# Performance work log

Measured on AMD Instinct MI355X. Metric: run time of the kernel, lower is better.

## Reference

```python
import jax, jax.numpy as jnp
import numpy as np

B = 4096   # per-view batch size
D = 256    # projection dim
TEMPERATURE = 0.1
EPS = 1e-12  # F.normalize eps


def setup_inputs() -> dict:
    key = jax.random.key(0)
    kq, kk = jax.random.split(key)
    features_q = jax.random.normal(kq, (B, D), dtype=jnp.float32)
    features_k = jax.random.normal(kk, (B, D), dtype=jnp.float32)
    return {"features_q": features_q, "features_k": features_k}


def _neg_index_matrix(n):
    # Static (numpy) construction of the per-row negative column indices:
    # row i keeps all columns except i (diagonal) and its positive partner.
    rows = np.arange(n)
    partner = (rows + n // 2) % n
    cols = np.broadcast_to(np.arange(n), (n, n))
    keep = (cols != rows[:, None]) & (cols != partner[:, None])
    return cols[keep].reshape(n, n - 2), partner


def reference(features_q, features_k):
    f = jnp.concatenate([features_q, features_k], axis=0)      # [2B, D]
    norm = jnp.maximum(jnp.linalg.norm(f, axis=1, keepdims=True), EPS)
    f = f / norm
    sim = f @ f.T                                              # [2B, 2B]

    n = 2 * B
    neg_idx_np, partner_np = _neg_index_matrix(n)
    rows = jnp.arange(n)
    partner = jnp.asarray(partner_np)
    pos = sim[rows, partner]                                   # [2B]
    neg = jnp.take_along_axis(sim, jnp.asarray(neg_idx_np), axis=1)  # [2B, 2B-2]

    logits = jnp.concatenate([pos[:, None], neg], axis=1) / TEMPERATURE
    # CrossEntropyLoss with label 0 for every row, mean reduction:
    loss = jnp.mean(jax.nn.logsumexp(logits, axis=1) - logits[:, 0])
    return loss
```

## Files before the change

### kernel.cpp

```cpp
#include <hip/hip_runtime.h>
#include <hip/hip_bf16.h>
#include <math.h>

#define N_TOTAL 8192
#define D_DIM   256
#define INV_T   10.0f
#define BM 128
#define BN 128
#define BK 32
#define K_ITERS (D_DIM / BK)
#define NT 64
#define N_TILES (NT * (NT + 1) / 2)

typedef __bf16 bf16_8 __attribute__((ext_vector_type(8)));
typedef float  f32x4  __attribute__((ext_vector_type(4)));

typedef const __attribute__((address_space(1))) unsigned int* gptr_t;
typedef __attribute__((address_space(3))) unsigned int*       lptr_t;

__device__ __forceinline__ void gload16(const void* g, void* l) {
    __builtin_amdgcn_global_load_lds((gptr_t)g, (lptr_t)l, 16, 0, 0);
}

__device__ __forceinline__ unsigned short f2bf(float f) {
    unsigned int u = __float_as_uint(f);
    return (unsigned short)((u + 0x7FFFu + ((u >> 16) & 1u)) >> 16);
}

__global__ __launch_bounds__(256) void normalize_kernel(
    const float* __restrict__ q, const float* __restrict__ k,
    unsigned short* __restrict__ F, float* __restrict__ out)
{
    if (blockIdx.x == 0 && threadIdx.x == 0) out[0] = 0.f;
    int row  = blockIdx.x * 4 + (threadIdx.x >> 6);
    int lane = threadIdx.x & 63;
    const float* src = (row < 4096) ? (q + (size_t)row * D_DIM)
                                    : (k + (size_t)(row - 4096) * D_DIM);
    float4 v = ((const float4*)src)[lane];
    float ss = v.x*v.x + v.y*v.y + v.z*v.z + v.w*v.w;
    #pragma unroll
    for (int off = 32; off > 0; off >>= 1) ss += __shfl_xor(ss, off, 64);
    float inv = 1.0f / fmaxf(sqrtf(ss), 1e-12f);
    ushort4 o;
    o.x = f2bf(v.x * inv); o.y = f2bf(v.y * inv);
    o.z = f2bf(v.z * inv); o.w = f2bf(v.w * inv);
    ((ushort4*)(F + (size_t)row * D_DIM))[lane] = o;
}

__device__ __forceinline__ int tri_off(int x) { return x * NT - (x * (x - 1)) / 2; }

__global__ __launch_bounds__(256) void simloss_gemm(
    const __hip_bfloat16* __restrict__ F,
    float* __restrict__ partial, float* __restrict__ pos)
{
    __shared__ __hip_bfloat16 As[2][BM * BK];
    __shared__ __hip_bfloat16 Bs[2][BN * BK];
    __shared__ float s_row[BM];
    __shared__ float s_col[BN];

    int b  = blockIdx.x;
    int bx = (int)(64.5f - sqrtf(64.5f * 64.5f - 2.0f * (float)b));
    if (bx < 0) bx = 0; if (bx > NT - 1) bx = NT - 1;
    while (bx > 0 && tri_off(bx) > b) --bx;
    while (bx < NT - 1 && tri_off(bx + 1) <= b) ++bx;
    const int by = bx + (b - tri_off(bx));
    const bool is_diag = (bx == by);

    const int i0 = bx * BM;
    const int j0 = by * BN;
    const int tid  = threadIdx.x;
    const int wave = tid >> 6;
    const int lane = tid & 63;
    const int wm = (wave & 1) * 64;
    const int wn = (wave >> 1) * 64;
    const int g  = lane >> 4;
    const int cj = lane & 15;
    const int srow  = lane >> 2;
    const int squar = (lane & 3) * 8;

    if (tid < BM) { s_row[tid] = 0.f; s_col[tid] = 0.f; }

    f32x4 acc[4][4];
    #pragma unroll
    for (int a = 0; a < 4; ++a)
        #pragma unroll
        for (int c = 0; c < 4; ++c)
            acc[a][c] = (f32x4){0.f, 0.f, 0.f, 0.f};

    #define STAGE(buf, kk)                                                            \
        _Pragma("unroll")                                                             \
        for (int p = 0; p < 2; ++p) {                                                 \
            gload16(F + (size_t)(i0 + wave * 32 + p * 16 + srow) * D_DIM + (kk) + squar, \
                    &As[buf][(wave * 32 + p * 16) * BK]);                             \
            gload16(F + (size_t)(j0 + wave * 32 + p * 16 + srow) * D_DIM + (kk) + squar, \
                    &Bs[buf][(wave * 32 + p * 16) * BK]);                             \
        }

    STAGE(0, 0);
    int cur = 0;
    for (int kk = 0; kk < K_ITERS; ++kk) {
        __builtin_amdgcn_s_barrier();
        if (kk + 1 < K_ITERS) {
            STAGE(cur ^ 1, (kk + 1) * BK);
            asm volatile("s_waitcnt vmcnt(4)" ::: "memory");
        } else {
            asm volatile("s_waitcnt vmcnt(0)" ::: "memory");
        }

        bf16_8 a[4], bfr[4];
        #pragma unroll
        for (int t = 0; t < 4; ++t) {
            a[t]   = *(const bf16_8*)(&As[cur][(wm + t * 16 + cj) * BK + g * 8]);
            bfr[t] = *(const bf16_8*)(&Bs[cur][(wn + t * 16 + cj) * BK + g * 8]);
        }
        #pragma unroll
        for (int ti = 0; ti < 4; ++ti)
            #pragma unroll
            for (int tj = 0; tj < 4; ++tj)
                acc[ti][tj] = __builtin_amdgcn_mfma_f32_16x16x32_bf16(
                    a[ti], bfr[tj], acc[ti][tj], 0, 0, 0);

        cur ^= 1;
    }
    #undef STAGE

    float colsum[4] = {0.f, 0.f, 0.f, 0.f};
    #pragma unroll
    for (int ti = 0; ti < 4; ++ti) {
        #pragma unroll
        for (int r = 0; r < 4; ++r) {
            const int i = i0 + wm + ti * 16 + g * 4 + r;
            const int partner = (i + 4096) & (N_TOTAL - 1);
            float esum = 0.f;
            #pragma unroll
            for (int tj = 0; tj < 4; ++tj) {
                const int j = j0 + wn + tj * 16 + cj;
                const float v = acc[ti][tj][r];
                float e = __expf(v * INV_T);
                if (is_diag && j == i) e = 0.f;
                if (!is_diag && j == partner) {
                    pos[i] = v; pos[j] = v;
                }
                esum += e;
                colsum[tj] += e;
            }
            #pragma unroll
            for (int off = 1; off < 16; off <<= 1)
                esum += __shfl_xor(esum, off, 64);
            if (cj == 0) atomicAdd(&s_row[wm + ti * 16 + g * 4 + r], esum);
        }
    }
    if (!is_diag) {
        #pragma unroll
        for (int tj = 0; tj < 4; ++tj) {
            float cs = colsum[tj];
            cs += __shfl_xor(cs, 16, 64);
            cs += __shfl_xor(cs, 32, 64);
            if (g == 0) atomicAdd(&s_col[wn + tj * 16 + cj], cs);
        }
    }
    __syncthreads();

    if (tid < BM) {
        partial[(size_t)by * N_TOTAL + i0 + tid] = s_row[tid];
    } else if (!is_diag) {
        partial[(size_t)bx * N_TOTAL + j0 + (tid - BM)] = s_col[tid - BM];
    }
}

__global__ __launch_bounds__(256) void finalize_kernel(
    const float* __restrict__ partial, const float* __restrict__ pos,
    float* __restrict__ out)
{
    const int row = blockIdx.x * 256 + threadIdx.x;
    float s = 0.f;
    #pragma unroll 8
    for (int t = 0; t < NT; ++t)
        s += partial[(size_t)t * N_TOTAL + row];
    float v = logf(s) - pos[row] * INV_T;
    #pragma unroll
    for (int off = 32; off > 0; off >>= 1) v += __shfl_xor(v, off, 64);
    __shared__ float wsum[4];
    if ((threadIdx.x & 63) == 0) wsum[threadIdx.x >> 6] = v;
    __syncthreads();
    if (threadIdx.x == 0)
        atomicAdd(out, (wsum[0] + wsum[1] + wsum[2] + wsum[3]) * (1.0f / N_TOTAL));
}

extern "C" void kernel_launch(void* const* d_in, const int* in_sizes, int n_in,
                              void* d_out, int out_size, void* d_ws, size_t ws_size,
                              hipStream_t stream) {
    const float* q = (const float*)d_in[0];
    const float* k = (const float*)d_in[1];
    float* out = (float*)d_out;

    char* ws = (char*)d_ws;
    const size_t f_bytes = (size_t)N_TOTAL * D_DIM * sizeof(unsigned short);
    const size_t p_bytes = (size_t)NT * N_TOTAL * sizeof(float);
    unsigned short* F = (unsigned short*)ws;
    float* partial = (float*)(ws + f_bytes);
    float* pos     = (float*)(ws + f_bytes + p_bytes);

    normalize_kernel<<<N_TOTAL / 4, 256, 0, stream>>>(q, k, F, out);
    simloss_gemm<<<N_TILES, 256, 0, stream>>>((const __hip_bfloat16*)F, partial, pos);
    finalize_kernel<<<32, 256, 0, stream>>>(partial, pos, out);
}
```

Before: 103.2 us.

## Fuse finalize into GEMM via per-panel completion counters and DPP row reductions

Removes the separate finalize kernel launch. Each GEMM block increments per-panel atomic counters, and the block that completes a panel sums its partials, computes the log-sum-exp loss terms and atomically accumulates the mean. The 16-lane row reduction switches from shuffles to DPP row-shift adds. This saves a launch and the tail kernel, but adds global fences, atomic counters and serial finalize work in the last blocks.

After: 251.7 us. 2.44x slower.

```diff
diff --git a/kernel.cpp b/kernel.cpp
--- a/kernel.cpp
+++ b/kernel.cpp
@@ -27,11 +27,28 @@
     return (unsigned short)((u + 0x7FFFu + ((u >> 16) & 1u)) >> 16);
 }
 
+template <int CTRL>
+__device__ __forceinline__ float dpp_add(float x) {
+    int y = __builtin_amdgcn_update_dpp(0, __float_as_int(x), CTRL, 0xf, 0xf, true);
+    return x + __int_as_float(y);
+}
+__device__ __forceinline__ float row16_sum(float x) {
+    x = dpp_add<0x111>(x);
+    x = dpp_add<0x112>(x);
+    x = dpp_add<0x114>(x);
+    x = dpp_add<0x118>(x);
+    return x;
+}
+
 __global__ __launch_bounds__(256) void normalize_kernel(
     const float* __restrict__ q, const float* __restrict__ k,
-    unsigned short* __restrict__ F, float* __restrict__ out)
+    unsigned short* __restrict__ F, float* __restrict__ out,
+    unsigned int* __restrict__ cnt)
 {
-    if (blockIdx.x == 0 && threadIdx.x == 0) out[0] = 0.f;
+    if (blockIdx.x == 0) {
+        if (threadIdx.x < 64) cnt[threadIdx.x] = 0u;
+        if (threadIdx.x == 0) out[0] = 0.f;
+    }
     int row  = blockIdx.x * 4 + (threadIdx.x >> 6);
     int lane = threadIdx.x & 63;
     const float* src = (row < 4096) ? (q + (size_t)row * D_DIM)
@@ -49,14 +66,36 @@
 
 __device__ __forceinline__ int tri_off(int x) { return x * NT - (x * (x - 1)) / 2; }
 
+__device__ __forceinline__ void panel_finalize(
+    int rx, const float* __restrict__ partial, const float* __restrict__ pos,
+    float* __restrict__ out, int tid)
+{
+    __threadfence();
+    float v = 0.f;
+    if (tid < BM) {
+        const int row = rx * BM + tid;
+        float s = 0.f;
+        #pragma unroll 8
+        for (int t = 0; t < NT; ++t)
+            s += partial[(size_t)t * N_TOTAL + row];
+        v = logf(s) - pos[row] * INV_T;
+    }
+    #pragma unroll
+    for (int off = 32; off > 0; off >>= 1) v += __shfl_xor(v, off, 64);
+    if ((tid & 63) == 0 && tid < BM)
+        atomicAdd(out, v * (1.0f / N_TOTAL));
+}
+
 __global__ __launch_bounds__(256) void simloss_gemm(
     const __hip_bfloat16* __restrict__ F,
-    float* __restrict__ partial, float* __restrict__ pos)
+    float* __restrict__ partial, float* __restrict__ pos,
+    unsigned int* __restrict__ cnt, float* __restrict__ out)
 {
     __shared__ __hip_bfloat16 As[2][BM * BK];
     __shared__ __hip_bfloat16 Bs[2][BN * BK];
     __shared__ float s_row[BM];
     __shared__ float s_col[BN];
+    __shared__ int s_flag[2];
 
     int b  = blockIdx.x;
     int bx = (int)(64.5f - sqrtf(64.5f * 64.5f - 2.0f * (float)b));
@@ -144,10 +183,8 @@
                 esum += e;
                 colsum[tj] += e;
             }
-            #pragma unroll
-            for (int off = 1; off < 16; off <<= 1)
-                esum += __shfl_xor(esum, off, 64);
-            if (cj == 0) atomicAdd(&s_row[wm + ti * 16 + g * 4 + r], esum);
+            esum = row16_sum(esum);
+            if (cj == 15) atomicAdd(&s_row[wm + ti * 16 + g * 4 + r], esum);
         }
     }
     if (!is_diag) {
@@ -166,25 +203,22 @@
     } else if (!is_diag) {
         partial[(size_t)bx * N_TOTAL + j0 + (tid - BM)] = s_col[tid - BM];
     }
-}
-
-__global__ __launch_bounds__(256) void finalize_kernel(
-    const float* __restrict__ partial, const float* __restrict__ pos,
-    float* __restrict__ out)
-{
-    const int row = blockIdx.x * 256 + threadIdx.x;
-    float s = 0.f;
-    #pragma unroll 8
-    for (int t = 0; t < NT; ++t)
-        s += partial[(size_t)t * N_TOTAL + row];
-    float v = logf(s) - pos[row] * INV_T;
-    #pragma unroll
-    for (int off = 32; off > 0; off >>= 1) v += __shfl_xor(v, off, 64);
-    __shared__ float wsum[4];
-    if ((threadIdx.x & 63) == 0) wsum[threadIdx.x >> 6] = v;
+
+    __threadfence();
     __syncthreads();
-    if (threadIdx.x == 0)
-        atomicAdd(out, (wsum[0] + wsum[1] + wsum[2] + wsum[3]) * (1.0f / N_TOTAL));
+    if (tid == 0) {
+        unsigned int c0 = atomicAdd(&cnt[bx], 1u);
+        s_flag[0] = (c0 == 63u) ? 1 : 0;
+        if (!is_diag) {
+            unsigned int c1 = atomicAdd(&cnt[by], 1u);
+            s_flag[1] = (c1 == 63u) ? 1 : 0;
+        } else {
+            s_flag[1] = 0;
+        }
+    }
+    __syncthreads();
+    if (s_flag[0]) panel_finalize(bx, partial, pos, out, tid);
+    if (s_flag[1]) panel_finalize(by, partial, pos, out, tid);
 }
 
 extern "C" void kernel_launch(void* const* d_in, const int* in_sizes, int n_in,
@@ -197,11 +231,12 @@
     char* ws = (char*)d_ws;
     const size_t f_bytes = (size_t)N_TOTAL * D_DIM * sizeof(unsigned short);
     const size_t p_bytes = (size_t)NT * N_TOTAL * sizeof(float);
+    const size_t pos_bytes = (size_t)N_TOTAL * sizeof(float);
     unsigned short* F = (unsigned short*)ws;
     float* partial = (float*)(ws + f_bytes);
     float* pos     = (float*)(ws + f_bytes + p_bytes);
-
-    normalize_kernel<<<N_TOTAL / 4, 256, 0, stream>>>(q, k, F, out);
-    simloss_gemm<<<N_TILES, 256, 0, stream>>>((const __hip_bfloat16*)F, partial, pos);
-    finalize_kernel<<<32, 256, 0, stream>>>(partial, pos, out);
-}
+    unsigned int* cnt = (unsigned int*)(ws + f_bytes + p_bytes + pos_bytes);
+
+    normalize_kernel<<<N_TOTAL / 4, 256, 0, stream>>>(q, k, F, out, cnt);
+    simloss_gemm<<<N_TILES, 256, 0, stream>>>((const __hip_bfloat16*)F, partial, pos, cnt, out);
+}
```
